# Performance work log

Hardware: AMD Instinct MI355X
Metric: run time of the kernel (lower is better)

## Reference

```python
import jax, jax.numpy as jnp
import numpy as np

B, S, H, KVH, D, HID = 2, 2048, 32, 8, 128, 4096
WINDOW = 512
EPS = 1e-5
SCALE = D ** -0.5
NEG = jnp.finfo(jnp.float32).min


def cohere_layernorm(x, w):
    # true LayerNorm (mean-subtracting), fp32 compute, weight, no bias
    xf = x.astype(jnp.float32)
    mu = jnp.mean(xf, axis=-1, keepdims=True)
    var = jnp.mean((xf - mu) ** 2, axis=-1, keepdims=True)
    return (w.astype(jnp.float32) * (xf - mu) * jax.lax.rsqrt(var + EPS)).astype(x.dtype)


def rotate_half_interleaved(x):
    # interleaved pairs: (x0,x1,x2,x3,...) -> (-x1,x0,-x3,x2,...)
    x1 = x[..., ::2]
    x2 = x[..., 1::2]
    return jnp.stack([-x2, x1], axis=-1).reshape(x.shape)


def setup_inputs() -> dict:
    key = jax.random.key(0)
    ks = jax.random.split(key, 6)
    hidden_states = jax.random.normal(ks[0], (B, S, HID), jnp.float32)
    position_ids = jnp.broadcast_to(jnp.arange(S, dtype=jnp.int32), (B, S))
    # rotary table with interleave-repeated frequencies (Cohere style)
    inv_freq = 1.0 / (10000.0 ** (jnp.arange(0, D, 2, dtype=jnp.float32) / D))
    freqs = jnp.arange(S, dtype=jnp.float32)[:, None] * inv_freq[None, :]  # [S, D/2]
    emb = jnp.repeat(freqs, 2, axis=-1)  # [S, D]
    cos, sin = jnp.cos(emb), jnp.sin(emb)
    std = 0.02
    # weights stored [in, out] so projection is x @ W
    wq = jax.random.normal(ks[1], (HID, H * D), jnp.float32) * std
    wk = jax.random.normal(ks[2], (HID, KVH * D), jnp.float32) * std
    wv = jax.random.normal(ks[3], (HID, KVH * D), jnp.float32) * std
    wo = jax.random.normal(ks[4], (H * D, HID), jnp.float32) * std
    q_norm_w = jnp.ones((D,), jnp.float32)
    k_norm_w = jnp.ones((D,), jnp.float32)
    return {"hidden_states": hidden_states, "position_ids": position_ids,
            "cos": cos, "sin": sin, "wq": wq, "wk": wk, "wv": wv, "wo": wo,
            "q_norm_w": q_norm_w, "k_norm_w": k_norm_w}


def reference(hidden_states, position_ids, cos, sin, wq, wk, wv, wo, q_norm_w, k_norm_w):
    q = (hidden_states @ wq).reshape(B, S, H, D)
    k = (hidden_states @ wk).reshape(B, S, KVH, D)
    v = (hidden_states @ wv).reshape(B, S, KVH, D)
    # QK LayerNorm over head_dim
    q = cohere_layernorm(q, q_norm_w)
    k = cohere_layernorm(k, k_norm_w)
    # interleaved RoPE; cos/sin gathered by position then broadcast over heads (unsqueeze_dim=2)
    c = cos[position_ids][:, :, None, :]  # [B, S, 1, D]
    s = sin[position_ids][:, :, None, :]
    q = q * c + rotate_half_interleaved(q) * s
    k = k * c + rotate_half_interleaved(k) * s
    # GQA: expand KV heads, attention in bhsd layout
    rep = H // KVH
    qh = jnp.transpose(q, (0, 2, 1, 3))                      # [B, H, S, D]
    kh = jnp.transpose(jnp.repeat(k, rep, axis=2), (0, 2, 1, 3))
    vh = jnp.transpose(jnp.repeat(v, rep, axis=2), (0, 2, 1, 3))
    scores = jnp.einsum('bhqd,bhkd->bhqk', qh, kh) * SCALE   # [B, H, S, S]
    i = jnp.arange(S)[:, None]
    j = jnp.arange(S)[None, :]
    mask = (i >= j) & (i - j < WINDOW)                       # causal + sliding window
    scores = jnp.where(mask[None, None], scores, NEG)
    attn = jax.nn.softmax(scores, axis=-1)
    out = jnp.einsum('bhqk,bhkd->bhqd', attn, vh)
    out = jnp.transpose(out, (0, 2, 1, 3)).reshape(B, S, H * D)
    return out @ wo
```

## Files before the change

kernel.cpp:

```cpp
#include <hip/hip_runtime.h>
#include <hip/hip_bf16.h>
#include <cstdio>
#include <cstdint>

#define B_    2
#define S_    2048
#define H_    32
#define KVH_  8
#define D_    128
#define HID_  4096
#define WIN_  512
#define NROW_ (B_*S_)
#define NKV_  2048
#define SCALE_ 0.08838834764831845f
#define SL2E_  0.12751744932973953f

typedef __attribute__((ext_vector_type(8))) __bf16 bf16x8;
typedef __attribute__((ext_vector_type(4))) __bf16 bf16x4;
typedef __attribute__((ext_vector_type(4))) float  f32x4;

#define GAS __attribute__((address_space(1)))
#define LAS __attribute__((address_space(3)))

__global__ __launch_bounds__(256) void prep_all(const float* __restrict__ hidden,
                                                const float* __restrict__ wq,
                                                const float* __restrict__ wk,
                                                const float* __restrict__ wv,
                                                const float* __restrict__ wo,
                                                __hip_bfloat16* __restrict__ hb,
                                                __hip_bfloat16* __restrict__ wqT,
                                                __hip_bfloat16* __restrict__ wkvT,
                                                __hip_bfloat16* __restrict__ woT) {
    __shared__ float t[32][33];
    const int bid = blockIdx.x;
    if (bid < 16384) {
        const int i = (bid * 256 + threadIdx.x) * 4;
        float4 v = *(const float4*)(hidden + i);
        __hip_bfloat162 a, b;
        a.x = __float2bfloat16(v.x); a.y = __float2bfloat16(v.y);
        b.x = __float2bfloat16(v.z); b.y = __float2bfloat16(v.w);
        *(__hip_bfloat162*)(hb + i)     = a;
        *(__hip_bfloat162*)(hb + i + 2) = b;
        return;
    }
    const int tx = threadIdx.x & 31, ty = threadIdx.x >> 5;
    const int id = bid - 16384;
    const float* src; __hip_bfloat16* dst; int C, idx;
    if (id < 16384)      { src = wq; dst = wqT;  C = 4096; idx = id; }
    else if (id < 20480) { src = wk; dst = wkvT; C = 1024; idx = id - 16384; }
    else if (id < 24576) { src = wv; dst = wkvT + (size_t)1024*HID_; C = 1024; idx = id - 20480; }
    else                 { src = wo; dst = woT;  C = 4096; idx = id - 24576; }
    const int ctiles = C >> 5;
    const int c0 = (idx % ctiles) * 32, r0 = (idx / ctiles) * 32;
    #pragma unroll
    for (int i = 0; i < 4; ++i)
        t[ty + 8*i][tx] = src[(size_t)(r0 + ty + 8*i) * C + c0 + tx];
    __syncthreads();
    #pragma unroll
    for (int i = 0; i < 4; ++i)
        dst[(size_t)(c0 + ty + 8*i) * HID_ + r0 + tx] = __float2bfloat16(t[tx][ty + 8*i]);
}

template <int FN, int OMODE>
__global__ __launch_bounds__(512, 2) void gemm_t(const __hip_bfloat16* __restrict__ A,
                                                 const __hip_bfloat16* __restrict__ Bt,
                                                 void* __restrict__ Cv, void* __restrict__ C2,
                                                 int M, int N, int K, int nbx) {
    constexpr int BN   = FN * 64;
    constexpr int BLD  = BN / 128;
    constexpr int SLOT = (256 + BN) * 32;
    __shared__ __align__(16) __hip_bfloat16 L[4 * SLOT];
    const int tid  = threadIdx.x;
    const int lane = tid & 63, w = tid >> 6;
    const int wm = w >> 2, wn = w & 3;
    const int lc = lane & 15, lg = lane >> 4;
    const int nwg = gridDim.x, cpx = nwg >> 3;
    const int bid = blockIdx.x;
    const int swz = (bid & 7) * cpx + (bid >> 3);
    const int by = swz / nbx, bx = swz - by * nbx;
    const size_t row0 = (size_t)by * 256, col0 = (size_t)bx * BN;
    const int nt = K >> 5;

    const int srow = tid >> 2;
    const int spc  = tid & 3;
    const int slx  = spc ^ ((srow >> 1) & 3);
    const __hip_bfloat16* Ab = A  + row0 * K;
    const __hip_bfloat16* Bb = Bt + col0 * K;

#define STGA(tile_) do {                                                                   \
    const int ss_ = (tile_) & 3;                                                           \
    const int kt_ = ((tile_) < nt) ? (tile_) : (nt - 1);  \
    _Pragma("unroll")                                                                      \
    for (int rh_ = 0; rh_ < 2; ++rh_)                                                      \
        __builtin_amdgcn_global_load_lds(                                                  \
            (const GAS void*)(Ab + (size_t)(rh_*128 + srow) * K + kt_*32 + slx*8),         \
            (LAS void*)&L[ss_*SLOT + rh_*4096 + w*512], 16, 0, 0);                         \
} while (0)

#define STGB(tile_) do {                                                                   \
    const int ss_ = (tile_) & 3;                                                           \
    const int kt_ = ((tile_) < nt) ? (tile_) : (nt - 1);                                   \
    _Pragma("unroll")                                                                      \
    for (int bh_ = 0; bh_ < BLD; ++bh_)                                                    \
        __builtin_amdgcn_global_load_lds(                                                  \
            (const GAS void*)(Bb + (size_t)(bh_*128 + srow) * K + kt_*32 + slx*8),         \
            (LAS void*)&L[ss_*SLOT + 8192 + bh_*4096 + w*512], 16, 0, 0);                  \
} while (0)

#define VMW2L() do {                                                                       \
    if constexpr (FN == 4) asm volatile("s_waitcnt vmcnt(8)" ::: "memory");                \
    else                   asm volatile("s_waitcnt vmcnt(6)" ::: "memory");                \
} while (0)

    f32x4 acc[2][4][FN] = {};
    bf16x8 afr0[4], afr1[4], bfr[FN];

    STGA(0); STGB(0); STGA(1); STGB(1); STGA(2); STGB(2);
    VMW2L();
    asm volatile("s_barrier" ::: "memory");

    for (int t = 0; t < nt; ++t) {
        const int s_ = t & 3;

        #pragma unroll
        for (int fn = 0; fn < FN; ++fn) {
            const int rB = wn*(FN*16) + fn*16 + lc;
            bfr[fn] = *(const bf16x8*)&L[s_*SLOT + 8192 + rB*32 + ((lg ^ ((rB >> 1) & 3)) * 8)];
        }
        #pragma unroll
        for (int fm = 0; fm < 4; ++fm) {
            const int rA = wm*128 + fm*16 + lc;
            afr0[fm] = *(const bf16x8*)&L[s_*SLOT + rA*32 + ((lg ^ ((rA >> 1) & 3)) * 8)];
        }
        __builtin_amdgcn_sched_barrier(0);
        #pragma unroll
        for (int fm = 0; fm < 4; ++fm) {
            const int rA = wm*128 + 64 + fm*16 + lc;
            afr1[fm] = *(const bf16x8*)&L[s_*SLOT + rA*32 + ((lg ^ ((rA >> 1) & 3)) * 8)];
        }
        STGA(t + 3);
        asm volatile("s_waitcnt lgkmcnt(4)" ::: "memory");
        __builtin_amdgcn_sched_barrier(0);
        __builtin_amdgcn_s_setprio(1);
        #pragma unroll
        for (int fm = 0; fm < 4; ++fm)
            #pragma unroll
            for (int fn = 0; fn < FN; ++fn)
                acc[0][fm][fn] = __builtin_amdgcn_mfma_f32_16x16x32_bf16(
                    afr0[fm], bfr[fn], acc[0][fm][fn], 0, 0, 0);
        __builtin_amdgcn_s_setprio(0);

        STGB(t + 3);
        asm volatile("s_waitcnt lgkmcnt(0)" ::: "memory");
        __builtin_amdgcn_sched_barrier(0);
        __builtin_amdgcn_s_setprio(1);
        #pragma unroll
        for (int fm = 0; fm < 4; ++fm)
            #pragma unroll
            for (int fn = 0; fn < FN; ++fn)
                acc[1][fm][fn] = __builtin_amdgcn_mfma_f32_16x16x32_bf16(
                    afr1[fm], bfr[fn], acc[1][fm][fn], 0, 0, 0);
        __builtin_amdgcn_s_setprio(0);
        VMW2L();
        asm volatile("s_barrier" ::: "memory");
    }
#undef STGA
#undef STGB
#undef VMW2L
    asm volatile("s_waitcnt vmcnt(0)" ::: "memory");

    if constexpr (OMODE == 0) {
        float* C = (float*)Cv;
        #pragma unroll
        for (int qm = 0; qm < 2; ++qm)
            #pragma unroll
            for (int fm = 0; fm < 4; ++fm)
                #pragma unroll
                for (int fn = 0; fn < FN; ++fn) {
                    const size_t col = col0 + wn*(FN*16) + fn*16 + lc;
                    #pragma unroll
                    for (int rr = 0; rr < 4; ++rr) {
                        const size_t row = row0 + wm*128 + qm*64 + fm*16 + lg*4 + rr;
                        C[row * N + col] = acc[qm][fm][fn][rr];
                    }
                }
    } else if constexpr (OMODE == 1) {
        __hip_bfloat16* C = (__hip_bfloat16*)Cv;
        #pragma unroll
        for (int qm = 0; qm < 2; ++qm)
            #pragma unroll
            for (int fm = 0; fm < 4; ++fm)
                #pragma unroll
                for (int fn = 0; fn < FN; ++fn) {
                    const size_t col = col0 + wn*(FN*16) + fn*16 + lc;
                    #pragma unroll
                    for (int rr = 0; rr < 4; ++rr) {
                        const size_t row = row0 + wm*128 + qm*64 + fm*16 + lg*4 + rr;
                        C[row * N + col] = __float2bfloat16(acc[qm][fm][fn][rr]);
                    }
                }
    } else {
        if (bx < 8) {
            __hip_bfloat16* C = (__hip_bfloat16*)Cv;
            #pragma unroll
            for (int qm = 0; qm < 2; ++qm)
                #pragma unroll
                for (int fm = 0; fm < 4; ++fm)
                    #pragma unroll
                    for (int fn = 0; fn < FN; ++fn) {
                        const size_t col = col0 + wn*32 + fn*16 + lc;
                        #pragma unroll
                        for (int rr = 0; rr < 4; ++rr) {
                            const size_t row = row0 + wm*128 + qm*64 + fm*16 + lg*4 + rr;
                            C[row * 1024 + col] = __float2bfloat16(acc[qm][fm][fn][rr]);
                        }
                    }
        } else {
            __hip_bfloat16* lt = (__hip_bfloat16*)L;
            __syncthreads();
            #pragma unroll
            for (int qm = 0; qm < 2; ++qm)
                #pragma unroll
                for (int fm = 0; fm < 4; ++fm)
                    #pragma unroll
                    for (int fn = 0; fn < FN; ++fn) {
                        const int cl = wn*32 + fn*16 + lc;
                        #pragma unroll
                        for (int rr = 0; rr < 4; ++rr) {
                            const int rl = wm*128 + qm*64 + fm*16 + lg*4 + rr;
                            lt[cl*264 + rl] = __float2bfloat16(acc[qm][fm][fn][rr]);
                        }
                    }
            __syncthreads();
            const int bb = (int)(row0 >> 11), s0 = (int)(row0 & 2047);
            const int g  = (int)((col0 - 1024) >> 7);
            __hip_bfloat16* vto = (__hip_bfloat16*)C2 + (((size_t)bb*KVH_ + g) * D_) * (size_t)S_;
            const int d = tid >> 2, sc0 = (tid & 3) * 64;
            #pragma unroll
            for (int j = 0; j < 64; j += 8) {
                bf16x8 v = *(const bf16x8*)&lt[d*264 + sc0 + j];
                *(bf16x8*)&vto[(size_t)d*S_ + s0 + sc0 + j] = v;
            }
        }
    }
}

template <int NH, int LD, int XOFF>
__global__ __launch_bounds__(256) void ln_rope(const __hip_bfloat16* __restrict__ x,
                                               const float* __restrict__ wln,
                                               const float* __restrict__ cosT,
                                               const float* __restrict__ sinT,
                                               const int* __restrict__ pids,
                                               __hip_bfloat16* __restrict__ out) {
    const int lane = threadIdx.x & 63, wv = threadIdx.x >> 6;
    const int r = blockIdx.x * 4 + wv;
    const int h = r % NH;
    const int bs = r / NH;
    const int b = bs / S_, s = bs % S_;
    const __hip_bfloat162 xv2 = *(const __hip_bfloat162*)(x + (size_t)bs * LD + XOFF + h*D_ + lane*2);
    const float x0 = __bfloat162float(xv2.x), x1 = __bfloat162float(xv2.y);
    float sum = x0 + x1;
    #pragma unroll
    for (int o = 32; o; o >>= 1) sum += __shfl_xor(sum, o);
    const float mu = sum * (1.f / D_);
    const float dx = x0 - mu, dy = x1 - mu;
    float vs = dx*dx + dy*dy;
    #pragma unroll
    for (int o = 32; o; o >>= 1) vs += __shfl_xor(vs, o);
    const float rs = rsqrtf(vs * (1.f / D_) + 1e-5f);
    const float2 w2 = *(const float2*)(wln + lane*2);
    const float y0 = w2.x * dx * rs, y1 = w2.y * dy * rs;
    const int p = pids[bs];
    const float2 c  = *(const float2*)(cosT + (size_t)p * D_ + lane*2);
    const float2 sn = *(const float2*)(sinT + (size_t)p * D_ + lane*2);
    __hip_bfloat162 ov;
    ov.x = __float2bfloat16(y0 * c.x - y1 * sn.x);
    ov.y = __float2bfloat16(y1 * c.y + y0 * sn.y);
    *(__hip_bfloat162*)(out + (((size_t)b * NH + h) * S_ + s) * D_ + lane*2) = ov;
}

static __device__ __forceinline__ int sigk_(int r) { return (r & 3) | ((r >> 1) & 4); }

__global__ __launch_bounds__(256) void attn_fwd(const __hip_bfloat16* __restrict__ qr,
                                                const __hip_bfloat16* __restrict__ kr,
                                                const __hip_bfloat16* __restrict__ vt,
                                                __hip_bfloat16* __restrict__ ao) {
    __shared__ __align__(16) __hip_bfloat16 Ksl[2][64*D_];
    __shared__ __align__(16) __hip_bfloat16 Vsl[2][D_*64];
    const int lane = threadIdx.x & 63, w = threadIdx.x >> 6;
    const int lq = lane & 15, lg = lane >> 4;
    const int blk = blockIdx.x;
    const int qt = blk >> 6;
    const int bh = blk & 63;
    const int h = bh & (H_-1), b = bh >> 5;
    const int g = h >> 2;
    const int q0 = qt*64 + w*16;
    const int q  = q0 + lq;

    const __hip_bfloat16* qbase = qr + (((size_t)b*H_ + h)*S_ + q0) * D_;
    const __hip_bfloat16* kbase = kr + ((size_t)b*KVH_ + g) * (size_t)S_ * D_;
    const __hip_bfloat16* vbase = vt + ((size_t)b*KVH_ + g) * (size_t)D_ * S_;

    const int srK = lane >> 4, scK = lane & 15;
    const int srV = lane >> 3, scV = lane & 7;

#define STAGE(nb, k0s) do {                                                              \
    _Pragma("unroll")                                                                    \
    for (int s_ = 0; s_ < 4; ++s_) {                                                     \
        const int rK_ = s_*16 + w*4 + srK;                                               \
        const __hip_bfloat16* srcK_ = kbase + (size_t)((k0s) + rK_)*D_                   \
                                      + ((scK ^ sigk_(rK_)) * 8);                        \
        __builtin_amdgcn_global_load_lds((const GAS void*)srcK_,                         \
            (LAS void*)&Ksl[nb][(s_*16 + w*4)*D_], 16, 0, 0);                            \
    }                                                                                    \
    _Pragma("unroll")                                                                    \
    for (int s_ = 0; s_ < 4; ++s_) {                                                     \
        const int dV_ = s_*32 + w*8 + srV;                                               \
        const __hip_bfloat16* srcV_ = vbase + (size_t)dV_*S_ + (k0s)                     \
                                      + ((scV ^ (dV_ & 7)) * 8);                         \
        __builtin_amdgcn_global_load_lds((const GAS void*)srcV_,                         \
            (LAS void*)&Vsl[nb][(s_*32 + w*8)*64], 16, 0, 0);                            \
    }                                                                                    \
} while (0)

    bf16x8 qf[4];
    #pragma unroll
    for (int kk = 0; kk < 4; ++kk)
        qf[kk] = *(const bf16x8*)(qbase + lq*D_ + kk*32 + lg*8);

    f32x4 o[8] = {};
    float m = -1e30f, l = 0.f;

    int kst = qt*64 - (WIN_ - 1); if (kst < 0) kst = 0; kst &= ~63;
    const int nt = qt + 1 - (kst >> 6);
    const int kldrow = 8*(lq >> 2) + (lq & 3);

    STAGE(0, kst);

    for (int t = 0; t < nt; ++t) {
        const int k0 = kst + t*64;
        const int buf = t & 1;
        if (t + 1 < nt) {
            STAGE((t + 1) & 1, k0 + 64);
            asm volatile("s_waitcnt vmcnt(8)" ::: "memory");
        } else {
            asm volatile("s_waitcnt vmcnt(0)" ::: "memory");
        }
        __builtin_amdgcn_s_barrier();

        f32x4 sc[2][2] = {};
        __builtin_amdgcn_s_setprio(1);
        #pragma unroll
        for (int kb = 0; kb < 2; ++kb)
            #pragma unroll
            for (int f = 0; f < 2; ++f) {
                const int rA = kb*32 + 4*f + kldrow;
                const __hip_bfloat16* kp = &Ksl[buf][rA*D_];
                #pragma unroll
                for (int kk = 0; kk < 4; ++kk) {
                    bf16x8 ka = *(const bf16x8*)(kp + (((kk*4 + lg) ^ sigk_(rA)) * 8));
                    sc[kb][f] = __builtin_amdgcn_mfma_f32_16x16x32_bf16(ka, qf[kk], sc[kb][f], 0, 0, 0);
                }
            }
        __builtin_amdgcn_s_setprio(0);

        const int dqk = q - (k0 + 8*lg);
        float pv[16];
        float mx = -INFINITY;
        #pragma unroll
        for (int kb = 0; kb < 2; ++kb)
            #pragma unroll
            for (int f = 0; f < 2; ++f)
                #pragma unroll
                for (int r = 0; r < 4; ++r) {
                    const int c = kb*32 + 4*f + r;
                    const int d = dqk - c;
                    float v = (d >= 0 && d < WIN_) ? sc[kb][f][r] * SL2E_ : -INFINITY;
                    pv[kb*8 + f*4 + r] = v;
                    mx = fmaxf(mx, v);
                }
        mx = fmaxf(mx, __shfl_xor(mx, 16));
        mx = fmaxf(mx, __shfl_xor(mx, 32));
        const float mn = fmaxf(m, mx);
        const float alpha = exp2f(m - mn);
        float ls = 0.f;
        union { bf16x8 v; __hip_bfloat16 e[8]; } pu[2];
        #pragma unroll
        for (int kb = 0; kb < 2; ++kb)
            #pragma unroll
            for (int j = 0; j < 8; ++j) {
                const float p = exp2f(pv[kb*8 + j] - mn);
                ls += p;
                pu[kb].e[j] = __float2bfloat16(p);
            }
        ls += __shfl_xor(ls, 16);
        ls += __shfl_xor(ls, 32);
        l = l * alpha + ls;
        m = mn;
        #pragma unroll
        for (int n = 0; n < 8; ++n) {
            o[n][0] *= alpha; o[n][1] *= alpha; o[n][2] *= alpha; o[n][3] *= alpha;
        }

        __builtin_amdgcn_s_setprio(1);
        #pragma unroll
        for (int kb = 0; kb < 2; ++kb)
            #pragma unroll
            for (int n = 0; n < 8; ++n) {
                const int dR = n*16 + lq;
                bf16x8 vf8 = *(const bf16x8*)(&Vsl[buf][dR*64] + (((kb*4 + lg) ^ (dR & 7)) * 8));
                o[n] = __builtin_amdgcn_mfma_f32_16x16x32_bf16(vf8, pu[kb].v, o[n], 0, 0, 0);
            }
        __builtin_amdgcn_s_setprio(0);

        if (t + 1 < nt) __builtin_amdgcn_s_barrier();
    }
#undef STAGE

    const float rinv = 1.f / l;
    #pragma unroll
    for (int n = 0; n < 8; ++n) {
        union { bf16x4 v; __hip_bfloat16 e[4]; } ov;
        #pragma unroll
        for (int r = 0; r < 4; ++r) ov.e[r] = __float2bfloat16(o[n][r] * rinv);
        *(bf16x4*)(ao + ((size_t)b*S_ + q)*(H_*D_) + h*D_ + n*16 + lg*4) = ov.v;
    }
}

extern "C" void kernel_launch(void* const* d_in, const int* in_sizes, int n_in,
                              void* d_out, int out_size, void* d_ws, size_t ws_size,
                              hipStream_t stream) {
    const float* hidden = (const float*)d_in[0];
    const int*   pids   = (const int*)  d_in[1];
    const float* cosT   = (const float*)d_in[2];
    const float* sinT   = (const float*)d_in[3];
    const float* wq     = (const float*)d_in[4];
    const float* wk     = (const float*)d_in[5];
    const float* wv     = (const float*)d_in[6];
    const float* wo     = (const float*)d_in[7];
    const float* qnw    = (const float*)d_in[8];
    const float* knw    = (const float*)d_in[9];
    float* out = (float*)d_out;

    char* base = (char*)d_ws;
    size_t off = 0;
    auto take = [&](size_t bytes) -> void* {
        void* q = base + off;
        off = (off + bytes + 255) & ~(size_t)255;
        return q;
    };
    __hip_bfloat16* qfb  = (__hip_bfloat16*)take((size_t)NROW_*HID_*2);
    __hip_bfloat16* kf   = (__hip_bfloat16*)take((size_t)NROW_*1024*2);
    __hip_bfloat16* hb   = (__hip_bfloat16*)take((size_t)NROW_*HID_*2);
    __hip_bfloat16* wqT  = (__hip_bfloat16*)take((size_t)HID_*HID_*2);
    __hip_bfloat16* wkvT = (__hip_bfloat16*)take((size_t)NKV_*HID_*2);
    __hip_bfloat16* woT  = (__hip_bfloat16*)take((size_t)HID_*HID_*2);
    __hip_bfloat16* qr   = (__hip_bfloat16*)take((size_t)B_*H_*S_*D_*2);
    __hip_bfloat16* kr   = (__hip_bfloat16*)take((size_t)B_*KVH_*S_*D_*2);
    __hip_bfloat16* vt   = (__hip_bfloat16*)take((size_t)B_*KVH_*S_*D_*2);
    __hip_bfloat16* ao   = qfb;

    if (off > ws_size) {
        fprintf(stderr, "WORKSPACE TOO SMALL: need %zu have %zu\n", off, ws_size);
        return;
    }

    prep_all<<<16384 + 40960, 256, 0, stream>>>(hidden, wq, wk, wv, wo, hb, wqT, wkvT, woT);

    gemm_t<4,1><<<(NROW_/256)*(HID_/256), 512, 0, stream>>>(hb, wqT,  qfb, nullptr, NROW_, HID_, HID_, HID_/256);
    gemm_t<2,2><<<(NROW_/256)*(NKV_/128), 512, 0, stream>>>(hb, wkvT, kf,  vt,      NROW_, NKV_, HID_, NKV_/128);

    ln_rope<H_,   HID_, 0><<<(B_*S_*H_)/4,   256, 0, stream>>>(qfb, qnw, cosT, sinT, pids, qr);
    ln_rope<KVH_, 1024, 0><<<(B_*S_*KVH_)/4, 256, 0, stream>>>(kf,  knw, cosT, sinT, pids, kr);

    attn_fwd<<<B_*H_*(S_/64), 256, 0, stream>>>(qr, kr, vt, ao);

    gemm_t<4,0><<<(NROW_/256)*(HID_/256), 512, 0, stream>>>(ao, woT, out, nullptr, NROW_, HID_, H_*D_, HID_/256);
}
```

Measured before the change: 483.3 us.

## Fuse Q layernorm+RoPE into attention and widen attention blocks to 128 queries

Q LayerNorm and interleaved RoPE now run inside the attention kernel, which reads raw Q straight from the projection output. This removes the separate Q ln_rope launch and its intermediate write and read. Attention blocks grow to 512 threads covering 128 query rows, so each K/V tile staged in shared memory serves twice as many queries. The cost is a separate output buffer instead of reusing qfb, plus more register pressure from the launch bound of 512 threads with 4 blocks.

Result: faster. 463.5 us, median of 2 (-4.1%).

```diff
diff --git a/kernel.cpp b/kernel.cpp
--- a/kernel.cpp
+++ b/kernel.cpp
@@ -89,7 +89,7 @@
 
 #define STGA(tile_) do {                                                                   \
     const int ss_ = (tile_) & 3;                                                           \
-    const int kt_ = ((tile_) < nt) ? (tile_) : (nt - 1);  \
+    const int kt_ = ((tile_) < nt) ? (tile_) : (nt - 1);                                   \
     _Pragma("unroll")                                                                      \
     for (int rh_ = 0; rh_ < 2; ++rh_)                                                      \
         __builtin_amdgcn_global_load_lds(                                                  \
@@ -121,7 +121,6 @@
 
     for (int t = 0; t < nt; ++t) {
         const int s_ = t & 3;
-
         #pragma unroll
         for (int fn = 0; fn < FN; ++fn) {
             const int rB = wn*(FN*16) + fn*16 + lc;
@@ -281,23 +280,27 @@
 
 static __device__ __forceinline__ int sigk_(int r) { return (r & 3) | ((r >> 1) & 4); }
 
-__global__ __launch_bounds__(256) void attn_fwd(const __hip_bfloat16* __restrict__ qr,
-                                                const __hip_bfloat16* __restrict__ kr,
-                                                const __hip_bfloat16* __restrict__ vt,
-                                                __hip_bfloat16* __restrict__ ao) {
+__global__ __launch_bounds__(512, 4) void attn_fwd(const __hip_bfloat16* __restrict__ qfb,
+                                                   const __hip_bfloat16* __restrict__ kr,
+                                                   const __hip_bfloat16* __restrict__ vt,
+                                                   const float* __restrict__ qnw,
+                                                   const float* __restrict__ cosT,
+                                                   const float* __restrict__ sinT,
+                                                   const int* __restrict__ pids,
+                                                   __hip_bfloat16* __restrict__ ao) {
     __shared__ __align__(16) __hip_bfloat16 Ksl[2][64*D_];
     __shared__ __align__(16) __hip_bfloat16 Vsl[2][D_*64];
-    const int lane = threadIdx.x & 63, w = threadIdx.x >> 6;
+    const int tid = threadIdx.x;
+    const int lane = tid & 63, w = tid >> 6;
     const int lq = lane & 15, lg = lane >> 4;
     const int blk = blockIdx.x;
-    const int qt = blk >> 6;
-    const int bh = blk & 63;
+    const int qt = blk & 15;
+    const int bh = blk >> 4;
     const int h = bh & (H_-1), b = bh >> 5;
     const int g = h >> 2;
-    const int q0 = qt*64 + w*16;
+    const int q0 = qt*128 + w*16;
     const int q  = q0 + lq;
 
-    const __hip_bfloat16* qbase = qr + (((size_t)b*H_ + h)*S_ + q0) * D_;
     const __hip_bfloat16* kbase = kr + ((size_t)b*KVH_ + g) * (size_t)S_ * D_;
     const __hip_bfloat16* vbase = vt + ((size_t)b*KVH_ + g) * (size_t)D_ * S_;
 
@@ -306,43 +309,86 @@
 
 #define STAGE(nb, k0s) do {                                                              \
     _Pragma("unroll")                                                                    \
-    for (int s_ = 0; s_ < 4; ++s_) {                                                     \
-        const int rK_ = s_*16 + w*4 + srK;                                               \
+    for (int s_ = 0; s_ < 2; ++s_) {                                                     \
+        const int rK_ = w*8 + s_*4 + srK;                                                \
         const __hip_bfloat16* srcK_ = kbase + (size_t)((k0s) + rK_)*D_                   \
                                       + ((scK ^ sigk_(rK_)) * 8);                        \
         __builtin_amdgcn_global_load_lds((const GAS void*)srcK_,                         \
-            (LAS void*)&Ksl[nb][(s_*16 + w*4)*D_], 16, 0, 0);                            \
+            (LAS void*)&Ksl[nb][(w*8 + s_*4)*D_], 16, 0, 0);                             \
     }                                                                                    \
     _Pragma("unroll")                                                                    \
-    for (int s_ = 0; s_ < 4; ++s_) {                                                     \
-        const int dV_ = s_*32 + w*8 + srV;                                               \
+    for (int s_ = 0; s_ < 2; ++s_) {                                                     \
+        const int dV_ = w*16 + s_*8 + srV;                                               \
         const __hip_bfloat16* srcV_ = vbase + (size_t)dV_*S_ + (k0s)                     \
                                       + ((scV ^ (dV_ & 7)) * 8);                         \
         __builtin_amdgcn_global_load_lds((const GAS void*)srcV_,                         \
-            (LAS void*)&Vsl[nb][(s_*32 + w*8)*64], 16, 0, 0);                            \
+            (LAS void*)&Vsl[nb][(w*16 + s_*8)*64], 16, 0, 0);                            \
     }                                                                                    \
 } while (0)
 
+    int kst = qt*128 - (WIN_ - 1); if (kst < 0) kst = 0; kst &= ~63;
+    const int nt = qt*2 + 2 - (kst >> 6);
+
+    union { bf16x8 v; __hip_bfloat16 e[8]; } qraw[4];
+    const __hip_bfloat16* qb2 = qfb + ((size_t)(b*S_ + q)) * HID_ + h*D_;
+    #pragma unroll
+    for (int kk = 0; kk < 4; ++kk)
+        qraw[kk].v = *(const bf16x8*)(qb2 + kk*32 + lg*8);
+    const int p = pids[b*S_ + q];
+
+    STAGE(0, kst);
+
+    float sum = 0.f;
+    #pragma unroll
+    for (int kk = 0; kk < 4; ++kk)
+        #pragma unroll
+        for (int j = 0; j < 8; ++j) sum += __bfloat162float(qraw[kk].e[j]);
+    sum += __shfl_xor(sum, 16); sum += __shfl_xor(sum, 32);
+    const float mu = sum * (1.f / D_);
+    float vsq = 0.f;
+    #pragma unroll
+    for (int kk = 0; kk < 4; ++kk)
+        #pragma unroll
+        for (int j = 0; j < 8; ++j) {
+            const float dxx = __bfloat162float(qraw[kk].e[j]) - mu;
+            vsq += dxx * dxx;
+        }
+    vsq += __shfl_xor(vsq, 16); vsq += __shfl_xor(vsq, 32);
+    const float rsq = rsqrtf(vsq * (1.f / D_) + 1e-5f);
+
     bf16x8 qf[4];
     #pragma unroll
-    for (int kk = 0; kk < 4; ++kk)
-        qf[kk] = *(const bf16x8*)(qbase + lq*D_ + kk*32 + lg*8);
+    for (int kk = 0; kk < 4; ++kk) {
+        const int d0 = kk*32 + lg*8;
+        float wl[8], cc[8], ss[8], y[8];
+        *(float4*)&wl[0] = *(const float4*)(qnw + d0);
+        *(float4*)&wl[4] = *(const float4*)(qnw + d0 + 4);
+        *(float4*)&cc[0] = *(const float4*)(cosT + (size_t)p*D_ + d0);
+        *(float4*)&cc[4] = *(const float4*)(cosT + (size_t)p*D_ + d0 + 4);
+        *(float4*)&ss[0] = *(const float4*)(sinT + (size_t)p*D_ + d0);
+        *(float4*)&ss[4] = *(const float4*)(sinT + (size_t)p*D_ + d0 + 4);
+        #pragma unroll
+        for (int j = 0; j < 8; ++j)
+            y[j] = wl[j] * (__bfloat162float(qraw[kk].e[j]) - mu) * rsq;
+        union { bf16x8 v; __hip_bfloat16 e[8]; } qo;
+        #pragma unroll
+        for (int mpair = 0; mpair < 4; ++mpair) {
+            qo.e[2*mpair]   = __float2bfloat16(y[2*mpair]   * cc[2*mpair]   - y[2*mpair+1] * ss[2*mpair]);
+            qo.e[2*mpair+1] = __float2bfloat16(y[2*mpair+1] * cc[2*mpair+1] + y[2*mpair]   * ss[2*mpair+1]);
+        }
+        qf[kk] = qo.v;
+    }
 
     f32x4 o[8] = {};
     float m = -1e30f, l = 0.f;
-
-    int kst = qt*64 - (WIN_ - 1); if (kst < 0) kst = 0; kst &= ~63;
-    const int nt = qt + 1 - (kst >> 6);
     const int kldrow = 8*(lq >> 2) + (lq & 3);
-
-    STAGE(0, kst);
 
     for (int t = 0; t < nt; ++t) {
         const int k0 = kst + t*64;
         const int buf = t & 1;
         if (t + 1 < nt) {
             STAGE((t + 1) & 1, k0 + 64);
-            asm volatile("s_waitcnt vmcnt(8)" ::: "memory");
+            asm volatile("s_waitcnt vmcnt(4)" ::: "memory");
         } else {
             asm volatile("s_waitcnt vmcnt(0)" ::: "memory");
         }
@@ -389,9 +435,9 @@
         for (int kb = 0; kb < 2; ++kb)
             #pragma unroll
             for (int j = 0; j < 8; ++j) {
-                const float p = exp2f(pv[kb*8 + j] - mn);
-                ls += p;
-                pu[kb].e[j] = __float2bfloat16(p);
+                const float pw = exp2f(pv[kb*8 + j] - mn);
+                ls += pw;
+                pu[kb].e[j] = __float2bfloat16(pw);
             }
         ls += __shfl_xor(ls, 16);
         ls += __shfl_xor(ls, 32);
@@ -450,15 +496,14 @@
         return q;
     };
     __hip_bfloat16* qfb  = (__hip_bfloat16*)take((size_t)NROW_*HID_*2);
+    __hip_bfloat16* ao   = (__hip_bfloat16*)take((size_t)NROW_*HID_*2);
     __hip_bfloat16* kf   = (__hip_bfloat16*)take((size_t)NROW_*1024*2);
     __hip_bfloat16* hb   = (__hip_bfloat16*)take((size_t)NROW_*HID_*2);
     __hip_bfloat16* wqT  = (__hip_bfloat16*)take((size_t)HID_*HID_*2);
     __hip_bfloat16* wkvT = (__hip_bfloat16*)take((size_t)NKV_*HID_*2);
     __hip_bfloat16* woT  = (__hip_bfloat16*)take((size_t)HID_*HID_*2);
-    __hip_bfloat16* qr   = (__hip_bfloat16*)take((size_t)B_*H_*S_*D_*2);
     __hip_bfloat16* kr   = (__hip_bfloat16*)take((size_t)B_*KVH_*S_*D_*2);
     __hip_bfloat16* vt   = (__hip_bfloat16*)take((size_t)B_*KVH_*S_*D_*2);
-    __hip_bfloat16* ao   = qfb;
 
     if (off > ws_size) {
         fprintf(stderr, "WORKSPACE TOO SMALL: need %zu have %zu\n", off, ws_size);
@@ -470,10 +515,9 @@
     gemm_t<4,1><<<(NROW_/256)*(HID_/256), 512, 0, stream>>>(hb, wqT,  qfb, nullptr, NROW_, HID_, HID_, HID_/256);
     gemm_t<2,2><<<(NROW_/256)*(NKV_/128), 512, 0, stream>>>(hb, wkvT, kf,  vt,      NROW_, NKV_, HID_, NKV_/128);
 
-    ln_rope<H_,   HID_, 0><<<(B_*S_*H_)/4,   256, 0, stream>>>(qfb, qnw, cosT, sinT, pids, qr);
-    ln_rope<KVH_, 1024, 0><<<(B_*S_*KVH_)/4, 256, 0, stream>>>(kf,  knw, cosT, sinT, pids, kr);
-
-    attn_fwd<<<B_*H_*(S_/64), 256, 0, stream>>>(qr, kr, vt, ao);
+    ln_rope<KVH_, 1024, 0><<<(B_*S_*KVH_)/4, 256, 0, stream>>>(kf, knw, cosT, sinT, pids, kr);
+
+    attn_fwd<<<B_*H_*(S_/128), 512, 0, stream>>>(qfb, kr, vt, qnw, cosT, sinT, pids, ao);
 
     gemm_t<4,0><<<(NROW_/256)*(HID_/256), 512, 0, stream>>>(ao, woT, out, nullptr, NROW_, HID_, H_*D_, HID_/256);
 }
```
